# Performance work log

Measured on AMD Instinct MI355X. Metric: run time of the kernel, lower is better.

## Reference

```python
import jax, jax.numpy as jnp
import numpy as np

B, S, H, L, HEADS, VOCAB, POS = 32, 240, 1024, 8, 16, 48, 240
D = H // HEADS


def setup_inputs() -> dict:
    key = jax.random.key(0)
    ks = jax.random.split(key, 20)
    p = lambda k, shape: jax.random.normal(k, shape, jnp.float32) * 0.02
    x = jax.random.normal(ks[0], (B, S, VOCAB), jnp.float32)
    lengths = jnp.sort(jax.random.randint(ks[1], (B,), 120, S + 1))[::-1]
    lengths = lengths.at[0].set(S)  # padded max length == S
    return {
        "x": x,
        "w_emb": p(ks[2], (VOCAB, H)),
        "p_emb": p(ks[3], (POS, H)),
        "Wq": p(ks[4], (L, H, H)), "bq": p(ks[5], (L, H)),
        "Wk": p(ks[6], (L, H, H)), "bk": p(ks[7], (L, H)),
        "Wv": p(ks[8], (L, H, H)), "bv": p(ks[9], (L, H)),
        "W1": p(ks[10], (L, H, H)), "b1": p(ks[11], (L, H)),
        "W2": p(ks[12], (L, H, H)), "b2": p(ks[13], (L, H)),
        "ln1_s": jnp.ones((L, H), jnp.float32), "ln1_b": jnp.zeros((L, H), jnp.float32),
        "ln2_s": jnp.ones((L, H), jnp.float32), "ln2_b": jnp.zeros((L, H), jnp.float32),
        "Wfc": p(ks[14], (H, 4)), "bfc": p(ks[15], (4,)),
        "lengths": lengths,
    }


def _ln(x, s, b):
    m = jnp.mean(x, -1, keepdims=True)
    v = jnp.mean((x - m) ** 2, -1, keepdims=True)
    return (x - m) / jnp.sqrt(v + 1e-5) * s + b


def reference(x, w_emb, p_emb, Wq, bq, Wk, bk, Wv, bv, W1, b1, W2, b2,
              ln1_s, ln1_b, ln2_s, ln2_b, Wfc, bfc, lengths):
    tokens = jnp.argmax(x, -1)                      # [B,S] argmax over feature dim (48)
    valid = jnp.arange(S)[None, :] < lengths[:, None]  # [B,S] query-row validity
    # pack/unpack zeros out embeddings at padded positions; pos-enc added everywhere
    z = w_emb[tokens] * valid[..., None].astype(jnp.float32) + p_emb[None, :S]
    causal = jnp.tril(jnp.ones((S, S), bool))
    scale = 1.0 / jnp.sqrt(jnp.float32(H))          # source divides by sqrt(hidden), not sqrt(d_head)
    for i in range(L):
        q = (z @ Wq[i] + bq[i]).reshape(B, S, HEADS, D)
        k = (z @ Wk[i] + bk[i]).reshape(B, S, HEADS, D)
        v = (z @ Wv[i] + bv[i]).reshape(B, S, HEADS, D)
        scores = jnp.einsum('bqhd,bkhd->bhqk', q, k) * scale
        scores = jnp.where(causal, scores, -jnp.inf)
        # softmax over causal keys; padded query rows are zeroed (torch NaN->0 path)
        atten = jax.nn.softmax(scores, -1) * valid[:, None, :, None].astype(jnp.float32)
        out = jnp.einsum('bhqk,bkhd->bqhd', atten, v).reshape(B, S, H)
        z1 = _ln(z + out, ln1_s[i], ln1_b[i])       # dropout off in eval
        ff = jax.nn.gelu(z1 @ W1[i] + b1[i], approximate=False) @ W2[i] + b2[i]
        z = _ln(z1 + ff, ln2_s[i], ln2_b[i])
    z2 = jnp.mean(z, axis=1)                        # mean-pool includes padded positions (faithful)
    return jax.nn.softmax(z2 @ Wfc + bfc, axis=-1)
```

## Files before the change

### kernel.cpp

```cpp
#include <hip/hip_runtime.h>
#include <hip/hip_bf16.h>

#define Bz 32
#define Sz 240
#define Hz 1024
#define Lz 8
#define NHEADS 16
#define NVOCAB 48
#define DHEAD 64
#define VT_STRIDE 264

typedef unsigned short u16;
typedef unsigned int u32;
typedef __attribute__((ext_vector_type(8))) short short8v;
typedef __attribute__((ext_vector_type(4))) float floatx4;

__device__ __forceinline__ int get_len(const int* __restrict__ L, int b) {
  return (L[1] == 0) ? L[2 * b] : L[b];
}
__device__ __forceinline__ u16 f2bf(float f) {
  u32 u = __float_as_uint(f);
  return (u16)((u + 0x7FFFu + ((u >> 16) & 1u)) >> 16);
}
__device__ __forceinline__ float bf2f(u16 s) {
  return __uint_as_float(((u32)s) << 16);
}
__device__ __forceinline__ void async_copy16(const u16* g, u16* l) {
  __builtin_amdgcn_global_load_lds(
      (const __attribute__((address_space(1))) u32*)g,
      (__attribute__((address_space(3))) u32*)l, 16, 0, 0);
}

__global__ __launch_bounds__(256) void embed_kernel(
    const float* __restrict__ x, const float* __restrict__ w_emb,
    const float* __restrict__ p_emb, const int* __restrict__ lengths,
    float* __restrict__ z, u16* __restrict__ z_bf) {
  int bs = blockIdx.x;
  int b = bs / Sz, s = bs % Sz;
  __shared__ int stok;
  if (threadIdx.x == 0) {
    const float* xr = x + (size_t)bs * NVOCAB;
    float best = xr[0]; int bi = 0;
    for (int j = 1; j < NVOCAB; ++j) {
      float v = xr[j];
      if (v > best) { best = v; bi = j; }
    }
    stok = bi;
  }
  __syncthreads();
  int tok = stok;
  float valid = (s < get_len(lengths, b)) ? 1.f : 0.f;
  const float* we = w_emb + (size_t)tok * Hz;
  const float* pe = p_emb + (size_t)s * Hz;
  size_t base = (size_t)bs * Hz;
  for (int h = threadIdx.x; h < Hz; h += blockDim.x) {
    float v = we[h] * valid + pe[h];
    z[base + h] = v;
    z_bf[base + h] = f2bf(v);
  }
}

__global__ __launch_bounds__(256) void bias_concat(
    const float* __restrict__ bq, const float* __restrict__ bk,
    const float* __restrict__ bv, float* __restrict__ dst) {
  int i = blockIdx.x * 256 + threadIdx.x;
  int l = i / 3072, c = i % 3072;
  float v = (c < 1024) ? bq[l * 1024 + c]
          : (c < 2048) ? bk[l * 1024 + c - 1024]
                       : bv[l * 1024 + c - 2048];
  dst[i] = v;
}

struct WconvArgs { const float* src[5]; u16* dst[5]; };
__global__ __launch_bounds__(256) void wconv5(WconvArgs a) {
  __shared__ u16 T[32][33];
  const float* W = a.src[blockIdx.z];
  u16* wt = a.dst[blockIdx.z];
  int bi = blockIdx.y, bj = blockIdx.x;
  int r = threadIdx.x >> 3, c4 = (threadIdx.x & 7) * 4;
  float4 w4 = *(const float4*)(W + (size_t)(bi * 32 + r) * Hz + bj * 32 + c4);
  T[r][c4 + 0] = f2bf(w4.x); T[r][c4 + 1] = f2bf(w4.y);
  T[r][c4 + 2] = f2bf(w4.z); T[r][c4 + 3] = f2bf(w4.w);
  __syncthreads();
  u32 lo = (u32)T[c4 + 0][r] | ((u32)T[c4 + 1][r] << 16);
  u32 hi = (u32)T[c4 + 2][r] | ((u32)T[c4 + 3][r] << 16);
  uint2 val; val.x = lo; val.y = hi;
  *(uint2*)(wt + (size_t)(bj * 32 + r) * Hz + bi * 32 + c4) = val;
}

template <bool OUTBF16, bool GELU, bool RESID>
__global__ __launch_bounds__(256) void gemm_mfma(
    const u16* __restrict__ A, const u16* __restrict__ Wt,
    const float* __restrict__ bias, const float* __restrict__ resid,
    void* __restrict__ Cv, int nco) {
  __shared__ u16 As[16384];
  __shared__ u16 Bs[16384];
  int tid = threadIdx.x;
  int xt = nco >> 7;
  int nwg = (int)gridDim.x;
  int id0 = blockIdx.x;
  int q = nwg >> 3, r = nwg & 7;
  int xcd = id0 & 7, off = id0 >> 3;
  int id = (xcd < r ? xcd * (q + 1) : r * (q + 1) + (xcd - r) * q) + off;
  int per = xt << 3;
  int g = id / per;
  int rr = id - g * per;
  int ys = 60 - (g << 3); ys = ys > 8 ? 8 : ys;
  int row0 = ((g << 3) + rr % ys) * 128;
  int col0 = (rr / ys) * 128;

  int w = tid >> 6, lane = tid & 63;
  int l15 = lane & 15, lq = lane >> 4;
  int wr = w >> 1, wc = w & 1;
  floatx4 acc[4][4] = {};

  const u16* gA0 = A + (size_t)(row0 + 32 * w + l15) * 1024 + 8 * lq;
  const u16* gA1 = gA0 + 16 * 1024;
  const u16* gB0 = Wt + (size_t)(col0 + 32 * w + l15) * 1024 + 8 * lq;
  const u16* gB1 = gB0 + 16 * 1024;
  int sbase = (2 * w) * 512;

  int afrag_off[4], bfrag_off[4];
#pragma unroll
  for (int i = 0; i < 4; ++i) {
    afrag_off[i] = (wr * 4 + i) * 512 + lq * 128 + l15 * 8;
    bfrag_off[i] = (wc * 4 + i) * 512 + lq * 128 + l15 * 8;
  }

  for (int k0 = 0; k0 < 1024; k0 += 128) {
#pragma unroll
    for (int c = 0; c < 4; ++c) {
      int kk = k0 + 32 * c;
      async_copy16(gA0 + kk, &As[c * 4096 + sbase]);
      async_copy16(gA1 + kk, &As[c * 4096 + sbase + 512]);
      async_copy16(gB0 + kk, &Bs[c * 4096 + sbase]);
      async_copy16(gB1 + kk, &Bs[c * 4096 + sbase + 512]);
    }
    __syncthreads();
#pragma unroll
    for (int kt = 0; kt < 4; ++kt) {
      short8v af[4], bf[4];
#pragma unroll
      for (int i = 0; i < 4; ++i)
        af[i] = *(const short8v*)(&As[kt * 4096 + afrag_off[i]]);
#pragma unroll
      for (int i = 0; i < 4; ++i)
        bf[i] = *(const short8v*)(&Bs[kt * 4096 + bfrag_off[i]]);
#pragma unroll
      for (int mi = 0; mi < 4; ++mi)
#pragma unroll
        for (int ni = 0; ni < 4; ++ni)
          acc[mi][ni] = __builtin_amdgcn_mfma_f32_16x16x32_bf16(
              af[mi], bf[ni], acc[mi][ni], 0, 0, 0);
    }
    __syncthreads();
  }

  int rowbase = row0 + wr * 64, colbase = col0 + wc * 64;
#pragma unroll
  for (int ni = 0; ni < 4; ++ni) {
    int col = colbase + ni * 16 + l15;
    float bcol = bias[col];
#pragma unroll
    for (int mi = 0; mi < 4; ++mi) {
      int rtop = rowbase + mi * 16 + lq * 4;
#pragma unroll
      for (int reg = 0; reg < 4; ++reg) {
        float vv = acc[mi][ni][reg] + bcol;
        if (RESID) vv += resid[(size_t)(rtop + reg) * nco + col];
        if (GELU) vv = 0.5f * vv * (1.f + erff(vv * 0.70710678118654752f));
        if (OUTBF16)
          ((u16*)Cv)[(size_t)(rtop + reg) * nco + col] = f2bf(vv);
        else
          ((float*)Cv)[(size_t)(rtop + reg) * nco + col] = vv;
      }
    }
  }
}

__global__ __launch_bounds__(256) void attention_kernel(
    const u16* __restrict__ qkv, const int* __restrict__ lengths,
    const float* __restrict__ zres, float* __restrict__ out) {
  const int LDQ = 3072;
  __shared__ u16 Vt[64 * VT_STRIDE];
  __shared__ u16 Pb[4][16 * 40];
  int hh = blockIdx.x & 1;
  int h = (blockIdx.x >> 1) & 15;
  int b = blockIdx.x >> 5;
  int tid = threadIdx.x;
  const size_t base = ((size_t)b * Sz) * LDQ + (size_t)h * DHEAD;
  const u16* qp = qkv + base;
  const u16* kp = qkv + base + 1024;
  const u16* vp = qkv + base + 2048;

  for (int idx = tid; idx < 256 * 16; idx += 256) {
    int key = idx >> 4, d4 = (idx & 15) * 4;
    uint2 vv;
    if (key < Sz) vv = *(const uint2*)(vp + (size_t)key * LDQ + d4);
    else { vv.x = 0u; vv.y = 0u; }
    Vt[(d4 + 0) * VT_STRIDE + key] = (u16)(vv.x & 0xFFFF);
    Vt[(d4 + 1) * VT_STRIDE + key] = (u16)(vv.x >> 16);
    Vt[(d4 + 2) * VT_STRIDE + key] = (u16)(vv.y & 0xFFFF);
    Vt[(d4 + 3) * VT_STRIDE + key] = (u16)(vv.y >> 16);
  }
  __syncthreads();

  int w = tid >> 6, lane = tid & 63;
  int qgroup = lane >> 4, qcol = lane & 15;
  int len_b = get_len(lengths, b);

  for (int qt = hh * 8 + w; qt < hh * 8 + 8 && qt < 15; qt += 4) {
    const u16* qrow = qp + (size_t)(qt * 16 + qcol) * LDQ;
    short8v aq0 = *(const short8v*)(qrow + qgroup * 8);
    short8v aq1 = *(const short8v*)(qrow + 32 + qgroup * 8);
    floatx4 o0 = {0.f, 0.f, 0.f, 0.f}, o1 = o0, o2 = o0, o3 = o0;
    float m_run[4] = {-1e30f, -1e30f, -1e30f, -1e30f};
    float l_run[4] = {0.f, 0.f, 0.f, 0.f};
    int nsteps = (qt + 2) >> 1;

    for (int st = 0; st < nsteps; ++st) {
      int t0 = 2 * st, t1 = 2 * st + 1;
      bool has1 = (t1 <= qt);
      floatx4 s0 = {0.f, 0.f, 0.f, 0.f};
      {
        const u16* kr = kp + (size_t)(t0 * 16 + qcol) * LDQ;
        short8v bk0 = *(const short8v*)(kr + qgroup * 8);
        short8v bk1 = *(const short8v*)(kr + 32 + qgroup * 8);
        s0 = __builtin_amdgcn_mfma_f32_16x16x32_bf16(aq0, bk0, s0, 0, 0, 0);
        s0 = __builtin_amdgcn_mfma_f32_16x16x32_bf16(aq1, bk1, s0, 0, 0, 0);
      }
      floatx4 s1 = {0.f, 0.f, 0.f, 0.f};
      if (has1) {
        const u16* kr = kp + (size_t)(t1 * 16 + qcol) * LDQ;
        short8v bk0 = *(const short8v*)(kr + qgroup * 8);
        short8v bk1 = *(const short8v*)(kr + 32 + qgroup * 8);
        s1 = __builtin_amdgcn_mfma_f32_16x16x32_bf16(aq0, bk0, s1, 0, 0, 0);
        s1 = __builtin_amdgcn_mfma_f32_16x16x32_bf16(aq1, bk1, s1, 0, 0, 0);
      }
      int kg0 = t0 * 16 + qcol, kg1 = t1 * 16 + qcol;
      float p0[4], p1[4];
#pragma unroll
      for (int rg = 0; rg < 4; ++rg) {
        int row_g = qt * 16 + qgroup * 4 + rg;
        float x0 = (kg0 <= row_g) ? s0[rg] * 0.03125f : -1e30f;
        float x1 = (has1 && kg1 <= row_g) ? s1[rg] * 0.03125f : -1e30f;
        float mx = fmaxf(x0, x1);
        mx = fmaxf(mx, __shfl_xor(mx, 1));
        mx = fmaxf(mx, __shfl_xor(mx, 2));
        mx = fmaxf(mx, __shfl_xor(mx, 4));
        mx = fmaxf(mx, __shfl_xor(mx, 8));
        float mnew = fmaxf(m_run[rg], mx);
        float alpha = __expf(m_run[rg] - mnew);
        float e0 = __expf(x0 - mnew);
        float e1 = __expf(x1 - mnew);
        float rs = e0 + e1;
        rs += __shfl_xor(rs, 1);
        rs += __shfl_xor(rs, 2);
        rs += __shfl_xor(rs, 4);
        rs += __shfl_xor(rs, 8);
        l_run[rg] = l_run[rg] * alpha + rs;
        m_run[rg] = mnew;
        o0[rg] *= alpha; o1[rg] *= alpha; o2[rg] *= alpha; o3[rg] *= alpha;
        p0[rg] = e0; p1[rg] = e1;
      }
#pragma unroll
      for (int rg = 0; rg < 4; ++rg) {
        int rl = qgroup * 4 + rg;
        Pb[w][rl * 40 + qcol] = f2bf(p0[rg]);
        Pb[w][rl * 40 + 16 + qcol] = f2bf(p1[rg]);
      }
      __asm__ volatile("s_waitcnt lgkmcnt(0)" ::: "memory");
      short8v pa = *(const short8v*)(&Pb[w][qcol * 40 + qgroup * 8]);
      int kb0 = st * 32 + qgroup * 8;
      short8v bv0 = *(const short8v*)(&Vt[(0 * 16 + qcol) * VT_STRIDE + kb0]);
      short8v bv1 = *(const short8v*)(&Vt[(1 * 16 + qcol) * VT_STRIDE + kb0]);
      short8v bv2 = *(const short8v*)(&Vt[(2 * 16 + qcol) * VT_STRIDE + kb0]);
      short8v bv3 = *(const short8v*)(&Vt[(3 * 16 + qcol) * VT_STRIDE + kb0]);
      o0 = __builtin_amdgcn_mfma_f32_16x16x32_bf16(pa, bv0, o0, 0, 0, 0);
      o1 = __builtin_amdgcn_mfma_f32_16x16x32_bf16(pa, bv1, o1, 0, 0, 0);
      o2 = __builtin_amdgcn_mfma_f32_16x16x32_bf16(pa, bv2, o2, 0, 0, 0);
      o3 = __builtin_amdgcn_mfma_f32_16x16x32_bf16(pa, bv3, o3, 0, 0, 0);
    }

#pragma unroll
    for (int rg = 0; rg < 4; ++rg) {
      int row_g = qt * 16 + qgroup * 4 + rg;
      float vmask = (row_g < len_b) ? (1.f / l_run[rg]) : 0.f;
      size_t ob = ((size_t)b * Sz + row_g) * Hz + (size_t)h * DHEAD + qcol;
      out[ob]      = zres[ob]      + o0[rg] * vmask;
      out[ob + 16] = zres[ob + 16] + o1[rg] * vmask;
      out[ob + 32] = zres[ob + 32] + o2[rg] * vmask;
      out[ob + 48] = zres[ob + 48] + o3[rg] * vmask;
    }
  }
}

__global__ __launch_bounds__(256) void add_ln_kernel(
    float* __restrict__ z, u16* __restrict__ z_bf, const float* __restrict__ r,
    const float* __restrict__ gamma, const float* __restrict__ beta) {
  int bs = blockIdx.x, tid = threadIdx.x;
  size_t base = (size_t)bs * Hz;
  __shared__ float sred[256];
  float4 v4 = *(const float4*)(r + base + tid * 4);
  float sum = v4.x + v4.y + v4.z + v4.w;
  sred[tid] = sum; __syncthreads();
  for (int off = 128; off > 0; off >>= 1) {
    if (tid < off) sred[tid] += sred[tid + off];
    __syncthreads();
  }
  float mean = sred[0] * (1.f / Hz); __syncthreads();
  float dx = v4.x - mean, dy = v4.y - mean, dz = v4.z - mean, dw = v4.w - mean;
  sred[tid] = dx * dx + dy * dy + dz * dz + dw * dw; __syncthreads();
  for (int off = 128; off > 0; off >>= 1) {
    if (tid < off) sred[tid] += sred[tid + off];
    __syncthreads();
  }
  float rstd = rsqrtf(sred[0] * (1.f / Hz) + 1e-5f);
  float4 g4 = *(const float4*)(gamma + tid * 4);
  float4 b4 = *(const float4*)(beta + tid * 4);
  float4 o;
  o.x = dx * rstd * g4.x + b4.x;
  o.y = dy * rstd * g4.y + b4.y;
  o.z = dz * rstd * g4.z + b4.z;
  o.w = dw * rstd * g4.w + b4.w;
  *(float4*)(z + base + tid * 4) = o;
  uint2 pk;
  pk.x = (u32)f2bf(o.x) | ((u32)f2bf(o.y) << 16);
  pk.y = (u32)f2bf(o.z) | ((u32)f2bf(o.w) << 16);
  *(uint2*)(z_bf + base + tid * 4) = pk;
}

__global__ __launch_bounds__(256) void pool1_kernel(
    const float* __restrict__ z, float* __restrict__ pooled) {
  int chunk = blockIdx.x, b = blockIdx.y, tid = threadIdx.x;
  int h = chunk * 128 + (tid & 127);
  int half = tid >> 7;
  __shared__ float sred[256];
  const float* zp = z + ((size_t)b * Sz + half * 120) * Hz + h;
  float s = 0.f;
  for (int i = 0; i < 120; ++i) s += zp[(size_t)i * Hz];
  sred[tid] = s; __syncthreads();
  if (tid < 128)
    pooled[(size_t)b * Hz + chunk * 128 + tid] =
        (sred[tid] + sred[tid + 128]) * (1.f / Sz);
}

__global__ __launch_bounds__(256) void pool2_kernel(
    const float* __restrict__ pooled, const float* __restrict__ Wfc,
    const float* __restrict__ bfc, float* __restrict__ out) {
  int b = blockIdx.x, tid = threadIdx.x;
  __shared__ float red[256][4];
  float acc[4] = {0.f, 0.f, 0.f, 0.f};
#pragma unroll
  for (int j = 0; j < 4; ++j) {
    int hh = tid * 4 + j;
    float z2 = pooled[(size_t)b * Hz + hh];
#pragma unroll
    for (int c = 0; c < 4; ++c) acc[c] += z2 * Wfc[hh * 4 + c];
  }
#pragma unroll
  for (int c = 0; c < 4; ++c) red[tid][c] = acc[c];
  __syncthreads();
  for (int off = 128; off > 0; off >>= 1) {
    if (tid < off)
#pragma unroll
      for (int c = 0; c < 4; ++c) red[tid][c] += red[tid + off][c];
    __syncthreads();
  }
  if (tid == 0) {
    float lg[4], m = -1e30f;
#pragma unroll
    for (int c = 0; c < 4; ++c) { lg[c] = red[0][c] + bfc[c]; m = fmaxf(m, lg[c]); }
    float s = 0.f;
#pragma unroll
    for (int c = 0; c < 4; ++c) { lg[c] = expf(lg[c] - m); s += lg[c]; }
    float inv = 1.f / s;
#pragma unroll
    for (int c = 0; c < 4; ++c) out[b * 4 + c] = lg[c] * inv;
  }
}

extern "C" void kernel_launch(void* const* d_in, const int* in_sizes, int n_in,
                              void* d_out, int out_size, void* d_ws, size_t ws_size,
                              hipStream_t stream) {
  const float* x     = (const float*)d_in[0];
  const float* w_emb = (const float*)d_in[1];
  const float* p_emb = (const float*)d_in[2];
  const float* Wq = (const float*)d_in[3];
  const float* bq = (const float*)d_in[4];
  const float* Wk = (const float*)d_in[5];
  const float* bk = (const float*)d_in[6];
  const float* Wv = (const float*)d_in[7];
  const float* bv = (const float*)d_in[8];
  const float* W1 = (const float*)d_in[9];
  const float* b1 = (const float*)d_in[10];
  const float* W2 = (const float*)d_in[11];
  const float* b2 = (const float*)d_in[12];
  const float* ln1s = (const float*)d_in[13];
  const float* ln1b = (const float*)d_in[14];
  const float* ln2s = (const float*)d_in[15];
  const float* ln2b = (const float*)d_in[16];
  const float* Wfc  = (const float*)d_in[17];
  const float* bfc  = (const float*)d_in[18];
  const int* lengths = (const int*)d_in[19];
  float* out = (float*)d_out;

  const size_t BSH = (size_t)Bz * Sz * Hz;
  float* z    = (float*)d_ws;
  float* ao   = z + BSH;
  u16* z_bf   = (u16*)(ao + BSH);
  u16* ffb    = z_bf + BSH;
  u16* qkv    = ffb + BSH;
  u16* wt     = qkv + 3 * BSH;
  float* bqkv = (float*)(wt + 5 * 1024 * 1024);
  float* pooled = bqkv + Lz * 3072;

  embed_kernel<<<Bz * Sz, 256, 0, stream>>>(x, w_emb, p_emb, lengths, z, z_bf);
  bias_concat<<<Lz * 3072 / 256, 256, 0, stream>>>(bq, bk, bv, bqkv);

  for (int i = 0; i < Lz; ++i) {
    size_t wo = (size_t)i * Hz * Hz, bo = (size_t)i * Hz;
    WconvArgs wa;
    wa.src[0] = Wq + wo; wa.src[1] = Wk + wo; wa.src[2] = Wv + wo;
    wa.src[3] = W1 + wo; wa.src[4] = W2 + wo;
    wa.dst[0] = wt;                     wa.dst[1] = wt + 1024 * 1024;
    wa.dst[2] = wt + 2 * 1024 * 1024;   wa.dst[3] = wt + 3 * 1024 * 1024;
    wa.dst[4] = wt + 4 * 1024 * 1024;
    wconv5<<<dim3(32, 32, 5), 256, 0, stream>>>(wa);

    gemm_mfma<true, false, false><<<60 * 24, 256, 0, stream>>>(
        z_bf, wt, bqkv + (size_t)i * 3072, nullptr, qkv, 3072);
    attention_kernel<<<Bz * NHEADS * 2, 256, 0, stream>>>(qkv, lengths, z, ao);
    add_ln_kernel<<<Bz * Sz, 256, 0, stream>>>(z, z_bf, ao, ln1s + bo, ln1b + bo);
    gemm_mfma<true, true, false><<<60 * 8, 256, 0, stream>>>(
        z_bf, wt + 3 * 1024 * 1024, b1 + bo, nullptr, ffb, 1024);
    gemm_mfma<false, false, true><<<60 * 8, 256, 0, stream>>>(
        ffb, wt + 4 * 1024 * 1024, b2 + bo, z, ao, 1024);
    add_ln_kernel<<<Bz * Sz, 256, 0, stream>>>(z, z_bf, ao, ln2s + bo, ln2b + bo);
  }
  pool1_kernel<<<dim3(8, Bz), 256, 0, stream>>>(z, pooled);
  pool2_kernel<<<Bz, 256, 0, stream>>>(pooled, Wfc, bfc, out);
}
```

Before: 2.418 ms.

## Double-buffer GEMM K loop with larger 256-row tiles and 512-thread blocks

Reworks the bf16 MFMA GEMM to use 512-thread workgroups computing 256xBN tiles (BN=256 for QKV, 128 for FFN). The K loop becomes a 64-wide step with double-buffered LDS, so the async copies for the next step are issued before the MFMAs on the current buffer. The aim is to hide global-to-LDS latency and improve data reuse per block. In exchange the grid gets smaller (360/240 blocks), the XCD-grouped tile swizzle becomes a simpler mapping, and LDS and register use go up.

Result: faster. 2.279 ms (-5.8%).

```diff
diff --git a/kernel.cpp b/kernel.cpp
--- a/kernel.cpp
+++ b/kernel.cpp
@@ -88,81 +88,88 @@
   *(uint2*)(wt + (size_t)(bj * 32 + r) * Hz + bi * 32 + c4) = val;
 }
 
-template <bool OUTBF16, bool GELU, bool RESID>
-__global__ __launch_bounds__(256) void gemm_mfma(
+template <int BN, bool OUTBF16, bool GELU, bool RESID>
+__global__ __launch_bounds__(512, 2) void gemm_mfma(
     const u16* __restrict__ A, const u16* __restrict__ Wt,
     const float* __restrict__ bias, const float* __restrict__ resid,
     void* __restrict__ Cv, int nco) {
-  __shared__ u16 As[16384];
-  __shared__ u16 Bs[16384];
+  constexpr int MT = (BN == 256) ? 8 : 4;
+  constexpr int WGC = (BN == 256) ? 4 : 2;
+  constexpr int BKT = BN * 32;
+  __shared__ u16 As[2][16384];
+  __shared__ u16 Bs[2][BN * 64];
   int tid = threadIdx.x;
-  int xt = nco >> 7;
   int nwg = (int)gridDim.x;
   int id0 = blockIdx.x;
-  int q = nwg >> 3, r = nwg & 7;
-  int xcd = id0 & 7, off = id0 >> 3;
-  int id = (xcd < r ? xcd * (q + 1) : r * (q + 1) + (xcd - r) * q) + off;
-  int per = xt << 3;
-  int g = id / per;
-  int rr = id - g * per;
-  int ys = 60 - (g << 3); ys = ys > 8 ? 8 : ys;
-  int row0 = ((g << 3) + rr % ys) * 128;
-  int col0 = (rr / ys) * 128;
+  int id = (id0 & 7) * (nwg >> 3) + (id0 >> 3);
+  int ncols = nco / BN;
+  int row0 = (id / ncols) * 256;
+  int col0 = (id % ncols) * BN;
 
   int w = tid >> 6, lane = tid & 63;
   int l15 = lane & 15, lq = lane >> 4;
-  int wr = w >> 1, wc = w & 1;
-  floatx4 acc[4][4] = {};
+  int wr = w / WGC, wc = w % WGC;
+  floatx4 acc[MT][4] = {};
 
   const u16* gA0 = A + (size_t)(row0 + 32 * w + l15) * 1024 + 8 * lq;
   const u16* gA1 = gA0 + 16 * 1024;
-  const u16* gB0 = Wt + (size_t)(col0 + 32 * w + l15) * 1024 + 8 * lq;
+  const u16* gB0 = Wt + (size_t)(col0 + (BN == 256 ? 32 : 16) * w + l15) * 1024 + 8 * lq;
   const u16* gB1 = gB0 + 16 * 1024;
-  int sbase = (2 * w) * 512;
-
-  int afrag_off[4], bfrag_off[4];
-#pragma unroll
-  for (int i = 0; i < 4; ++i) {
-    afrag_off[i] = (wr * 4 + i) * 512 + lq * 128 + l15 * 8;
-    bfrag_off[i] = (wc * 4 + i) * 512 + lq * 128 + l15 * 8;
-  }
-
-  for (int k0 = 0; k0 < 1024; k0 += 128) {
-#pragma unroll
-    for (int c = 0; c < 4; ++c) {
-      int kk = k0 + 32 * c;
-      async_copy16(gA0 + kk, &As[c * 4096 + sbase]);
-      async_copy16(gA1 + kk, &As[c * 4096 + sbase + 512]);
-      async_copy16(gB0 + kk, &Bs[c * 4096 + sbase]);
-      async_copy16(gB1 + kk, &Bs[c * 4096 + sbase + 512]);
-    }
-    __syncthreads();
-#pragma unroll
-    for (int kt = 0; kt < 4; ++kt) {
-      short8v af[4], bf[4];
-#pragma unroll
-      for (int i = 0; i < 4; ++i)
-        af[i] = *(const short8v*)(&As[kt * 4096 + afrag_off[i]]);
-#pragma unroll
-      for (int i = 0; i < 4; ++i)
-        bf[i] = *(const short8v*)(&Bs[kt * 4096 + bfrag_off[i]]);
-#pragma unroll
-      for (int mi = 0; mi < 4; ++mi)
+
+  auto stage = [&](int bb, int kk) {
+#pragma unroll
+    for (int kt = 0; kt < 2; ++kt) {
+      async_copy16(gA0 + kk + 32 * kt, &As[bb][kt * 8192 + (2 * w) * 512]);
+      async_copy16(gA1 + kk + 32 * kt, &As[bb][kt * 8192 + (2 * w + 1) * 512]);
+      if constexpr (BN == 256) {
+        async_copy16(gB0 + kk + 32 * kt, &Bs[bb][kt * BKT + (2 * w) * 512]);
+        async_copy16(gB1 + kk + 32 * kt, &Bs[bb][kt * BKT + (2 * w + 1) * 512]);
+      } else {
+        async_copy16(gB0 + kk + 32 * kt, &Bs[bb][kt * BKT + w * 512]);
+      }
+    }
+  };
+
+  int afrag_off[MT], bfrag_off[4];
+#pragma unroll
+  for (int i = 0; i < MT; ++i)
+    afrag_off[i] = (wr * MT + i) * 512 + lq * 128 + l15 * 8;
+#pragma unroll
+  for (int j = 0; j < 4; ++j)
+    bfrag_off[j] = (wc * 4 + j) * 512 + lq * 128 + l15 * 8;
+
+  stage(0, 0);
+  __syncthreads();
+  int cur = 0;
+  for (int k0 = 0; k0 < 1024; k0 += 64) {
+    if (k0 + 64 < 1024) stage(cur ^ 1, k0 + 64);
+#pragma unroll
+    for (int kt = 0; kt < 2; ++kt) {
+      short8v af[MT], bf[4];
+#pragma unroll
+      for (int i = 0; i < MT; ++i)
+        af[i] = *(const short8v*)(&As[cur][kt * 8192 + afrag_off[i]]);
+#pragma unroll
+      for (int j = 0; j < 4; ++j)
+        bf[j] = *(const short8v*)(&Bs[cur][kt * BKT + bfrag_off[j]]);
+#pragma unroll
+      for (int mi = 0; mi < MT; ++mi)
 #pragma unroll
         for (int ni = 0; ni < 4; ++ni)
           acc[mi][ni] = __builtin_amdgcn_mfma_f32_16x16x32_bf16(
               af[mi], bf[ni], acc[mi][ni], 0, 0, 0);
     }
     __syncthreads();
-  }
-
-  int rowbase = row0 + wr * 64, colbase = col0 + wc * 64;
+    cur ^= 1;
+  }
+
+  int rowbase = row0 + wr * (MT * 16), colbase = col0 + wc * 64;
 #pragma unroll
   for (int ni = 0; ni < 4; ++ni) {
     int col = colbase + ni * 16 + l15;
     float bcol = bias[col];
 #pragma unroll
-    for (int mi = 0; mi < 4; ++mi) {
+    for (int mi = 0; mi < MT; ++mi) {
       int rtop = rowbase + mi * 16 + lq * 4;
 #pragma unroll
       for (int reg = 0; reg < 4; ++reg) {
@@ -428,13 +435,13 @@
     wa.dst[4] = wt + 4 * 1024 * 1024;
     wconv5<<<dim3(32, 32, 5), 256, 0, stream>>>(wa);
 
-    gemm_mfma<true, false, false><<<60 * 24, 256, 0, stream>>>(
+    gemm_mfma<256, true, false, false><<<30 * 12, 512, 0, stream>>>(
         z_bf, wt, bqkv + (size_t)i * 3072, nullptr, qkv, 3072);
     attention_kernel<<<Bz * NHEADS * 2, 256, 0, stream>>>(qkv, lengths, z, ao);
     add_ln_kernel<<<Bz * Sz, 256, 0, stream>>>(z, z_bf, ao, ln1s + bo, ln1b + bo);
-    gemm_mfma<true, true, false><<<60 * 8, 256, 0, stream>>>(
+    gemm_mfma<128, true, true, false><<<30 * 8, 512, 0, stream>>>(
         z_bf, wt + 3 * 1024 * 1024, b1 + bo, nullptr, ffb, 1024);
-    gemm_mfma<false, false, true><<<60 * 8, 256, 0, stream>>>(
+    gemm_mfma<128, false, false, true><<<30 * 8, 512, 0, stream>>>(
         ffb, wt + 4 * 1024 * 1024, b2 + bo, z, ao, 1024);
     add_ln_kernel<<<Bz * Sz, 256, 0, stream>>>(z, z_bf, ao, ln2s + bo, ln2b + bo);
   }
```
